# Optimization experiments

Measured on AMD Instinct MI355X. Metric: run time of the kernel, lower is better.

## Reference

```python
import jax, jax.numpy as jnp
import numpy as np

EMBED_DIM = 256
NUM_HEADS = 4
LN_EPS = 1e-5


def setup_inputs() -> dict:
    b, n, e = 2, 4096, EMBED_DIM
    key = jax.random.key(0)
    ks = jax.random.split(key, 12)
    x = jax.random.normal(ks[0], (b, n, e), dtype=jnp.float32)
    # rotary cache: cos/sin of random angles, shape [2, b, n, e, 1]
    ang = jax.random.uniform(ks[1], (b, n, e, 1), dtype=jnp.float32) * (2 * np.pi)
    encoding = jnp.stack([jnp.cos(ang), jnp.sin(ang)], axis=0)
    s_e = 1.0 / np.sqrt(e)
    s_2e = 1.0 / np.sqrt(2 * e)
    Wqkv_w = jax.random.normal(ks[2], (3 * e, e), dtype=jnp.float32) * s_e
    Wqkv_b = jax.random.normal(ks[3], (3 * e,), dtype=jnp.float32) * s_e
    out_w = jax.random.normal(ks[4], (e, e), dtype=jnp.float32) * s_e
    out_b = jax.random.normal(ks[5], (e,), dtype=jnp.float32) * s_e
    ffn1_w = jax.random.normal(ks[6], (2 * e, 2 * e), dtype=jnp.float32) * s_2e
    ffn1_b = jax.random.normal(ks[7], (2 * e,), dtype=jnp.float32) * s_2e
    ln_g = jnp.ones((2 * e,), dtype=jnp.float32)
    ln_b = jnp.zeros((2 * e,), dtype=jnp.float32)
    ffn2_w = jax.random.normal(ks[8], (e, 2 * e), dtype=jnp.float32) * s_2e
    ffn2_b = jax.random.normal(ks[9], (e,), dtype=jnp.float32) * s_2e
    return {"x": x, "encoding": encoding, "Wqkv_w": Wqkv_w, "Wqkv_b": Wqkv_b,
            "out_w": out_w, "out_b": out_b, "ffn1_w": ffn1_w, "ffn1_b": ffn1_b,
            "ln_g": ln_g, "ln_b": ln_b, "ffn2_w": ffn2_w, "ffn2_b": ffn2_b}


def _forward(x, encoding, Wqkv_w, Wqkv_b, out_w, out_b, ffn1_w, ffn1_b, ln_g, ln_b, ffn2_w, ffn2_b):
    b, n, e = x.shape
    h = NUM_HEADS
    hd = e // h
    qkv = x @ Wqkv_w.T + Wqkv_b                      # [b,n,3e]
    qkv = qkv.reshape(b, n, e, 3)
    qk, v = qkv[..., :2], qkv[..., 2]                # [b,n,e,2], [b,n,e]
    # rotate_half: interpret e as (h, hd//2, 2) pairs, rotate within pairs
    r = qk.reshape(b, n, h, hd // 2, 2, 2)
    r = jnp.stack([-r[..., 1, :], r[..., 0, :]], axis=4).reshape(b, n, e, 2)
    qk = qk * encoding[0] + r * encoding[1]          # cached rotary emb
    q = qk[..., 0].reshape(b, n, h, hd)
    k = qk[..., 1].reshape(b, n, h, hd)
    vh = v.reshape(b, n, h, hd)
    scale = 1.0 / np.sqrt(hd).astype(np.float32)
    scores = jnp.einsum('bqhd,bkhd->bhqk', q, k) * scale
    attn = jax.nn.softmax(scores, axis=-1)
    ctx = jnp.einsum('bhqk,bkhd->bqhd', attn, vh).reshape(b, n, e)
    message = ctx @ out_w.T + out_b
    y = jnp.concatenate([x, message], axis=2)        # [b,n,2e]
    y = y @ ffn1_w.T + ffn1_b
    mu = jnp.mean(y, axis=-1, keepdims=True)
    var = jnp.mean(jnp.square(y - mu), axis=-1, keepdims=True)
    y = (y - mu) * jax.lax.rsqrt(var + LN_EPS) * ln_g + ln_b
    y = jax.nn.gelu(y, approximate=False)            # torch nn.GELU default = exact
    y = y @ ffn2_w.T + ffn2_b
    return x + y


def reference(x, encoding, Wqkv_w, Wqkv_b, out_w, out_b, ffn1_w, ffn1_b, ln_g, ln_b, ffn2_w, ffn2_b):
    return _forward(x, encoding, Wqkv_w, Wqkv_b, out_w, out_b, ffn1_w, ffn1_b, ln_g, ln_b, ffn2_w, ffn2_b)
```

## Files before the change

kernel.cpp:

```cpp
#include <hip/hip_runtime.h>
#include <hip/hip_bf16.h>

using u16 = unsigned short;
using u16x8 = __attribute__((ext_vector_type(8))) unsigned short;
using s16x4 = __attribute__((ext_vector_type(4))) short;
using s16x8 = __attribute__((ext_vector_type(8))) short;
using f32x4 = __attribute__((ext_vector_type(4))) float;

__device__ __forceinline__ f32x4 mfma16(s16x8 a, s16x8 b, f32x4 c) {
    return __builtin_amdgcn_mfma_f32_16x16x32_bf16(a, b, c, 0, 0, 0);
}

__device__ __forceinline__ u16 f2bf(float f) {
    union { float f; unsigned u; } v; v.f = f;
    unsigned r = v.u + 0x7FFFu + ((v.u >> 16) & 1u);
    return (u16)(r >> 16);
}

__device__ __forceinline__ unsigned cvt_pk_bf16(float lo, float hi) {
    unsigned r;
    asm("v_cvt_pk_bf16_f32 %0, %1, %2" : "=v"(r) : "v"(lo), "v"(hi));
    return r;
}

__device__ __forceinline__ float fast_exp2(float x) {
    float r;
    asm("v_exp_f32 %0, %1" : "=v"(r) : "v"(x));
    return r;
}

__device__ __forceinline__ unsigned pk2(u16 a, u16 b) {
    return (unsigned)a | ((unsigned)b << 16);
}

__device__ __forceinline__ float bf2f(u16 u) {
    union { unsigned u; float f; } v; v.u = ((unsigned)u) << 16;
    return v.f;
}

__device__ __forceinline__ void gload_lds16(const u16* g, u16* l) {
    __builtin_amdgcn_global_load_lds(
        (const __attribute__((address_space(1))) void*)g,
        (__attribute__((address_space(3))) void*)l, 16, 0, 0);
}

__global__ __launch_bounds__(256) void conv_kernel(
    const float* __restrict__ s0, const float* __restrict__ s1,
    const float* __restrict__ s2, const float* __restrict__ s3,
    const float* __restrict__ s4,
    u16* __restrict__ d0, u16* __restrict__ d1, u16* __restrict__ d2,
    u16* __restrict__ d3, u16* __restrict__ d4)
{
    int i = blockIdx.x * 256 + threadIdx.x;
    const float* s; u16* d; int off;
    if (i < 524288)      { s = s0; d = d0; off = i; }
    else if (i < 573440) { s = s1; d = d1; off = i - 524288; }
    else if (i < 589824) { s = s2; d = d2; off = i - 573440; }
    else if (i < 655360) { s = s3; d = d3; off = i - 589824; }
    else                 { s = s4; d = d4; off = i - 655360; }
    float4 f = ((const float4*)s)[off];
    ushort4 u;
    u.x = f2bf(f.x); u.y = f2bf(f.y); u.z = f2bf(f.z); u.w = f2bf(f.w);
    ((ushort4*)d)[off] = u;
}

template<int OUTMODE, bool SPLIT, bool RESID>
__global__ __launch_bounds__(256) void gemm_kernel(
    const u16* __restrict__ A0, const u16* __restrict__ A1,
    const u16* __restrict__ W, const float* __restrict__ bias,
    const float* __restrict__ resid, float* __restrict__ outf,
    u16* __restrict__ outb, int M, int N, int K)
{
    __shared__ u16 A_lds[128][72];
    __shared__ u16 B_lds[64][72];
    const int tid = threadIdx.x;
    const int l = tid & 63, w = tid >> 6;
    const int lr = l & 15, lg = l >> 4;
    const int m0 = blockIdx.x * 128, n0 = blockIdx.y * 64;
    const int wm = (w >> 1) * 64, wn = (w & 1) * 32;

    f32x4 acc[4][2];
    #pragma unroll
    for (int i = 0; i < 4; ++i)
        #pragma unroll
        for (int j = 0; j < 2; ++j)
            acc[i][j] = (f32x4){0.f, 0.f, 0.f, 0.f};

    for (int k0 = 0; k0 < K; k0 += 64) {
        __syncthreads();
        const u16* Asrc; int lda;
        if (SPLIT) {
            lda = 256;
            Asrc = (k0 < 256) ? (A0 + k0) : (A1 + (k0 - 256));
        } else {
            lda = K; Asrc = A0 + k0;
        }
        #pragma unroll
        for (int i = 0; i < 4; ++i) {
            int c = tid + 256 * i;
            int row = c >> 3, cg = c & 7;
            *(uint4*)&A_lds[row][cg * 8] =
                *(const uint4*)(Asrc + (size_t)(m0 + row) * lda + cg * 8);
        }
        #pragma unroll
        for (int i = 0; i < 2; ++i) {
            int c = tid + 256 * i;
            int row = c >> 3, cg = c & 7;
            *(uint4*)&B_lds[row][cg * 8] =
                *(const uint4*)(W + (size_t)(n0 + row) * K + k0 + cg * 8);
        }
        __syncthreads();
        #pragma unroll
        for (int ks = 0; ks < 2; ++ks) {
            s16x8 af[4], bfr[2];
            #pragma unroll
            for (int ms = 0; ms < 4; ++ms)
                af[ms] = *(const s16x8*)&A_lds[wm + ms * 16 + lr][ks * 32 + lg * 8];
            #pragma unroll
            for (int ns = 0; ns < 2; ++ns)
                bfr[ns] = *(const s16x8*)&B_lds[wn + ns * 16 + lr][ks * 32 + lg * 8];
            #pragma unroll
            for (int ms = 0; ms < 4; ++ms)
                #pragma unroll
                for (int ns = 0; ns < 2; ++ns)
                    acc[ms][ns] = mfma16(af[ms], bfr[ns], acc[ms][ns]);
        }
    }
    #pragma unroll
    for (int ms = 0; ms < 4; ++ms) {
        #pragma unroll
        for (int ns = 0; ns < 2; ++ns) {
            int cg = n0 + wn + ns * 16 + lr;
            float bv = bias[cg];
            #pragma unroll
            for (int r = 0; r < 4; ++r) {
                int rg = m0 + wm + ms * 16 + lg * 4 + r;
                float val = acc[ms][ns][r] + bv;
                if (RESID) val += resid[(size_t)rg * N + cg];
                if (OUTMODE == 0) outf[(size_t)rg * N + cg] = val;
                else              outb[(size_t)rg * N + cg] = f2bf(val);
            }
        }
    }
}

__global__ __launch_bounds__(256) void rope_kernel(
    const u16* __restrict__ qkv, const float* __restrict__ enc,
    u16* __restrict__ Qo, u16* __restrict__ Ko, u16* __restrict__ Vo)
{
    int idx = blockIdx.x * 256 + threadIdx.x;
    int row = idx >> 7;
    int p = idx & 127;
    int c0 = p * 2;
    const u16* base = qkv + (size_t)row * 768 + p * 6;
    ushort2 a01 = *(const ushort2*)(base);
    ushort2 a23 = *(const ushort2*)(base + 2);
    ushort2 a45 = *(const ushort2*)(base + 4);
    float q0 = bf2f(a01.x), k0 = bf2f(a01.y);
    float q1 = bf2f(a23.y), k1 = bf2f(a45.x);
    const float* cb = enc + (size_t)row * 256 + c0;
    float2 cosv = *(const float2*)cb;
    float2 sinv = *(const float2*)(cb + 2097152);
    float qr0 = q0 * cosv.x - q1 * sinv.x;
    float qr1 = q1 * cosv.y + q0 * sinv.y;
    float kr0 = k0 * cosv.x - k1 * sinv.x;
    float kr1 = k1 * cosv.y + k0 * sinv.y;
    const float qs = 0.18033688011112042f;
    qr0 *= qs; qr1 *= qs;
    int h = c0 >> 6, d = c0 & 63;
    int b = row >> 12, n = row & 4095;
    size_t o = (((size_t)(b * 4 + h)) * 4096 + n) * 64 + d;
    *(unsigned*)(Qo + o) = cvt_pk_bf16(qr0, qr1);
    *(unsigned*)(Ko + o) = cvt_pk_bf16(kr0, kr1);
    *(unsigned*)(Vo + o) = pk2(a23.x, a45.y);
}

__global__ __launch_bounds__(256) void transpose_v(
    const u16* __restrict__ V, u16* __restrict__ Vt)
{
    __shared__ u16 t[64][72];
    int bh = blockIdx.y, n0 = blockIdx.x * 64;
    int tid = threadIdx.x;
    #pragma unroll
    for (int i = 0; i < 2; ++i) {
        int c = tid + 256 * i;
        int r = c >> 3, cg = c & 7;
        *(uint4*)&t[r][cg * 8] =
            *(const uint4*)(V + ((size_t)bh * 4096 + n0 + r) * 64 + cg * 8);
    }
    __syncthreads();
    #pragma unroll
    for (int i = 0; i < 2; ++i) {
        int c = tid + 256 * i;
        int d = c >> 3, ng = c & 7;
        unsigned w0 = pk2(t[ng*8+0][d], t[ng*8+1][d]);
        unsigned w1 = pk2(t[ng*8+2][d], t[ng*8+3][d]);
        unsigned w2 = pk2(t[ng*8+4][d], t[ng*8+5][d]);
        unsigned w3 = pk2(t[ng*8+6][d], t[ng*8+7][d]);
        uint4 o4 = make_uint4(w0, w1, w2, w3);
        *(uint4*)(Vt + ((size_t)bh * 64 + d) * 4096 + n0 + ng * 8) = o4;
    }
}

__global__ __launch_bounds__(256) void attn_kernel(
    const u16* __restrict__ Qp, const u16* __restrict__ Kp,
    const u16* __restrict__ Vtp, u16* __restrict__ Opart,
    float* __restrict__ Ssum)
{
    __shared__ u16 K_lds[2][64][64];
    __shared__ u16 V_lds[2][64][64];
    const int tid = threadIdx.x;
    const int l = tid & 63, w = tid >> 6;
    const int lr = l & 15, lg = l >> 4;
    const int bh = blockIdx.y, z = blockIdx.z;
    const int n0 = blockIdx.x * 64 + w * 16;

    const u16* Qb = Qp + ((size_t)bh * 4096 + n0) * 64;
    s16x8 qf0 = *(const s16x8*)(Qb + lr * 64 + lg * 8);
    s16x8 qf1 = *(const s16x8*)(Qb + lr * 64 + 32 + lg * 8);

    const u16* Kb = Kp + (size_t)bh * 4096 * 64 + (size_t)z * 1024 * 64;
    const u16* Vb = Vtp + (size_t)bh * 64 * 4096 + z * 1024;

    const int swz = (l & 7) ^ ((l >> 3) & 7);
    const int row0 = 16 * w + (l >> 3);
    const size_t koff0 = (size_t)row0 * 64 + swz * 8;
    const size_t koff1 = (size_t)(row0 + 8) * 64 + swz * 8;
    const size_t voff0 = (size_t)row0 * 4096 + swz * 8;
    const size_t voff1 = (size_t)(row0 + 8) * 4096 + swz * 8;

    #define STAGE(kt, b)                                                      \
        do {                                                                  \
            const u16* ks_ = Kb + (size_t)(kt) * 4096;                        \
            const u16* vs_ = Vb + (size_t)(kt) * 64;                          \
            gload_lds16(ks_ + koff0, &K_lds[b][16 * w][0]);                   \
            gload_lds16(ks_ + koff1, &K_lds[b][16 * w + 8][0]);               \
            gload_lds16(vs_ + voff0, &V_lds[b][16 * w][0]);                   \
            gload_lds16(vs_ + voff1, &V_lds[b][16 * w + 8][0]);               \
        } while (0)

    f32x4 O[4];
    #pragma unroll
    for (int dv = 0; dv < 4; ++dv) O[dv] = (f32x4){0.f, 0.f, 0.f, 0.f};
    f32x4 ssum = (f32x4){0.f, 0.f, 0.f, 0.f};
    s16x8 ones;
    #pragma unroll
    for (int j = 0; j < 8; ++j) ones[j] = (short)0x3F80;

    const int r7 = lr & 7;

    STAGE(0, 0);
    __syncthreads();

    for (int kt = 0; kt < 16; ++kt) {
        const int cur = kt & 1;
        if (kt + 1 < 16) STAGE(kt + 1, cur ^ 1);

        f32x4 S[4];
        #pragma unroll
        for (int v4 = 0; v4 < 4; ++v4) {
            const int krow = v4 * 16 + lr;
            s16x8 kf0 = *(const s16x8*)&K_lds[cur][krow][(lg ^ r7) * 8];
            s16x8 kf1 = *(const s16x8*)&K_lds[cur][krow][((4 + lg) ^ r7) * 8];
            f32x4 zz = (f32x4){-24.f, -24.f, -24.f, -24.f};
            zz = mfma16(kf0, qf0, zz);
            zz = mfma16(kf1, qf1, zz);
            S[v4] = zz;
        }

        float p[4][4];
        #pragma unroll
        for (int v4 = 0; v4 < 4; ++v4)
            #pragma unroll
            for (int r = 0; r < 4; ++r)
                p[v4][r] = fast_exp2(S[v4][r]);

        s16x8 pa[2];
        #pragma unroll
        for (int kb = 0; kb < 2; ++kb) {
            union { unsigned u[4]; s16x8 v; } pu;
            pu.u[0] = cvt_pk_bf16(p[2*kb][0],   p[2*kb][1]);
            pu.u[1] = cvt_pk_bf16(p[2*kb][2],   p[2*kb][3]);
            pu.u[2] = cvt_pk_bf16(p[2*kb+1][0], p[2*kb+1][1]);
            pu.u[3] = cvt_pk_bf16(p[2*kb+1][2], p[2*kb+1][3]);
            pa[kb] = pu.v;
        }

        #pragma unroll
        for (int dv = 0; dv < 4; ++dv) {
            const int vrow = 16 * dv + lr;
            #pragma unroll
            for (int kb = 0; kb < 2; ++kb) {
                const int c16a = 4 * kb + (lg >> 1);
                const u16* vpa = &V_lds[cur][vrow][((c16a      ^ r7) * 8) + 4 * (lg & 1)];
                const u16* vpb = &V_lds[cur][vrow][(((c16a + 2) ^ r7) * 8) + 4 * (lg & 1)];
                s16x4 va  = *(const s16x4*)vpa;
                s16x4 vb4 = *(const s16x4*)vpb;
                s16x8 vf = __builtin_shufflevector(va, vb4, 0,1,2,3,4,5,6,7);
                O[dv] = mfma16(pa[kb], vf, O[dv]);
            }
        }
        ssum = mfma16(pa[0], ones, ssum);
        ssum = mfma16(pa[1], ones, ssum);

        __syncthreads();
    }
    #undef STAGE

    u16* Ob = Opart + ((size_t)(z * 8 + bh) * 4096 + n0) * 64;
    #pragma unroll
    for (int dv = 0; dv < 4; ++dv)
        #pragma unroll
        for (int r = 0; r < 4; ++r)
            Ob[(size_t)(4 * lg + r) * 64 + 16 * dv + lr] = f2bf(O[dv][r]);
    if (lr == 0) {
        float4 sv = make_float4(ssum[0], ssum[1], ssum[2], ssum[3]);
        *(float4*)&Ssum[(size_t)(z * 8 + bh) * 4096 + n0 + 4 * lg] = sv;
    }
}

__global__ __launch_bounds__(256) void combine_kernel(
    const u16* __restrict__ Opart, const float* __restrict__ Ssum,
    u16* __restrict__ ctx)
{
    int idx = blockIdx.x * 256 + threadIdx.x;
    int rr = idx >> 3;
    int dc = (idx & 7) * 8;
    float s = Ssum[rr] + Ssum[32768 + rr] + Ssum[65536 + rr] + Ssum[98304 + rr];
    float inv = 1.f / s;
    float acc[8];
    #pragma unroll
    for (int j = 0; j < 8; ++j) acc[j] = 0.f;
    #pragma unroll
    for (int z = 0; z < 4; ++z) {
        u16x8 ov = *(const u16x8*)(Opart + ((size_t)z * 32768 + rr) * 64 + dc);
        #pragma unroll
        for (int j = 0; j < 8; ++j) acc[j] += bf2f(ov[j]);
    }
    #pragma unroll
    for (int j = 0; j < 8; ++j) acc[j] *= inv;
    int bh = rr >> 12, n = rr & 4095;
    int b = bh >> 2, h = bh & 3;
    uint4 o4 = make_uint4(cvt_pk_bf16(acc[0], acc[1]), cvt_pk_bf16(acc[2], acc[3]),
                          cvt_pk_bf16(acc[4], acc[5]), cvt_pk_bf16(acc[6], acc[7]));
    *(uint4*)(ctx + ((size_t)(b * 4096 + n)) * 256 + h * 64 + dc) = o4;
}

__global__ __launch_bounds__(256) void ln_gelu_kernel(
    const float* __restrict__ y, const float* __restrict__ g,
    const float* __restrict__ bta, u16* __restrict__ o)
{
    int row = blockIdx.x * 4 + (threadIdx.x >> 6);
    int l = threadIdx.x & 63;
    const float* yr = y + (size_t)row * 512 + l * 8;
    float4 va = *(const float4*)yr;
    float4 vb = *(const float4*)(yr + 4);
    float v[8] = {va.x, va.y, va.z, va.w, vb.x, vb.y, vb.z, vb.w};
    float s = 0.f;
    #pragma unroll
    for (int j = 0; j < 8; ++j) s += v[j];
    #pragma unroll
    for (int off = 32; off; off >>= 1) s += __shfl_xor(s, off, 64);
    float mu = s * (1.f / 512.f);
    float q = 0.f;
    #pragma unroll
    for (int j = 0; j < 8; ++j) { float t = v[j] - mu; q += t * t; }
    #pragma unroll
    for (int off = 32; off; off >>= 1) q += __shfl_xor(q, off, 64);
    float rs = rsqrtf(q * (1.f / 512.f) + 1e-5f);
    u16 u[8];
    #pragma unroll
    for (int j = 0; j < 8; ++j) {
        float t = (v[j] - mu) * rs * g[l * 8 + j] + bta[l * 8 + j];
        t = t * 0.5f * (1.f + erff(t * 0.70710678118654752f));
        u[j] = f2bf(t);
    }
    uint4 o4 = make_uint4(pk2(u[0], u[1]), pk2(u[2], u[3]),
                          pk2(u[4], u[5]), pk2(u[6], u[7]));
    *(uint4*)(o + (size_t)row * 512 + l * 8) = o4;
}

extern "C" void kernel_launch(void* const* d_in, const int* in_sizes, int n_in,
                              void* d_out, int out_size, void* d_ws, size_t ws_size,
                              hipStream_t stream) {
    (void)in_sizes; (void)n_in; (void)out_size; (void)ws_size;
    const float* x    = (const float*)d_in[0];
    const float* enc  = (const float*)d_in[1];
    const float* wqkv = (const float*)d_in[2];
    const float* bqkv = (const float*)d_in[3];
    const float* wout = (const float*)d_in[4];
    const float* bout = (const float*)d_in[5];
    const float* w1   = (const float*)d_in[6];
    const float* b1   = (const float*)d_in[7];
    const float* lng  = (const float*)d_in[8];
    const float* lnb  = (const float*)d_in[9];
    const float* w2   = (const float*)d_in[10];
    const float* b2   = (const float*)d_in[11];
    float* out = (float*)d_out;
    char* ws = (char*)d_ws;

    u16*   xb    = (u16*)(ws + 0);
    u16*   wqkvb = (u16*)(ws + 4194304);
    u16*   woutb = (u16*)(ws + 4587520);
    u16*   w1b   = (u16*)(ws + 4718592);
    u16*   w2b   = (u16*)(ws + 5242880);
    u16*   qkvb  = (u16*)(ws + 5505024);
    u16*   OpartB= (u16*)(ws + 5505024);
    float* y1    = (float*)(ws + 5505024);
    float* Ssum  = (float*)(ws + 22282240);
    u16*   q     = (u16*)(ws + 30670848);
    u16*   k     = (u16*)(ws + 34865152);
    u16*   v     = (u16*)(ws + 39059456);
    u16*   vt    = (u16*)(ws + 43253760);
    u16*   ybf   = q;
    u16*   ctx   = (u16*)(ws + 47448064);
    u16*   msg   = (u16*)(ws + 51642368);

    conv_kernel<<<2688, 256, 0, stream>>>(x, wqkv, wout, w1, w2,
                                          xb, wqkvb, woutb, w1b, w2b);
    gemm_kernel<1, false, false><<<dim3(64, 12), 256, 0, stream>>>(
        xb, nullptr, wqkvb, bqkv, nullptr, nullptr, qkvb, 8192, 768, 256);
    rope_kernel<<<4096, 256, 0, stream>>>(qkvb, enc, q, k, v);
    transpose_v<<<dim3(64, 8), 256, 0, stream>>>(v, vt);
    attn_kernel<<<dim3(64, 8, 4), 256, 0, stream>>>(q, k, vt, OpartB, Ssum);
    combine_kernel<<<1024, 256, 0, stream>>>(OpartB, Ssum, ctx);
    gemm_kernel<1, false, false><<<dim3(64, 4), 256, 0, stream>>>(
        ctx, nullptr, woutb, bout, nullptr, nullptr, msg, 8192, 256, 256);
    gemm_kernel<0, true, false><<<dim3(64, 8), 256, 0, stream>>>(
        xb, msg, w1b, b1, nullptr, y1, nullptr, 8192, 512, 512);
    ln_gelu_kernel<<<2048, 256, 0, stream>>>(y1, lng, lnb, ybf);
    gemm_kernel<0, false, true><<<dim3(64, 4), 256, 0, stream>>>(
        ybf, nullptr, w2b, b2, x, out, nullptr, 8192, 256, 512);
}
```

Before: 139.4 us.

## Triple-buffer LDS with async global-to-LDS loads in GEMM and attention

The GEMM kernel moves from synchronous register-staged loads with two barriers per k-step to direct global-to-LDS async loads into a 3-deep XOR-swizzled ring buffer, prefetching the next stage and using vmcnt waits plus a single barrier per iteration. The attention kernel goes from double to triple buffering of K/V tiles and drops the trailing barrier. The aim is to overlap memory latency with MFMA work and cut synchronisation. The cost is more LDS per block, which may lower occupancy. Correctness with one barrier also depends on the exact vmcnt counts and the ring depth.

New measurement: 135.3 us. -2.9%, faster.

```diff
diff --git a/kernel.cpp b/kernel.cpp
--- a/kernel.cpp
+++ b/kernel.cpp
@@ -71,14 +71,38 @@
     const float* __restrict__ resid, float* __restrict__ outf,
     u16* __restrict__ outb, int M, int N, int K)
 {
-    __shared__ u16 A_lds[128][72];
-    __shared__ u16 B_lds[64][72];
+    __shared__ u16 A_lds[3][128][64];
+    __shared__ u16 B_lds[3][64][64];
     const int tid = threadIdx.x;
     const int l = tid & 63, w = tid >> 6;
     const int lr = l & 15, lg = l >> 4;
+    const int r7 = lr & 7;
     const int m0 = blockIdx.x * 128, n0 = blockIdx.y * 64;
     const int wm = (w >> 1) * 64, wn = (w & 1) * 32;
 
+    const int lrow = l >> 3;
+    const int swz = (l & 7) ^ lrow;
+    const int arow = 32 * w + lrow;
+    const int brow = 16 * w + lrow;
+
+    #define STAGE_G(s, b)                                                     \
+        do {                                                                  \
+            int k0_ = 64 * (s);                                               \
+            const u16* As_; int lda_;                                         \
+            if (SPLIT) {                                                      \
+                lda_ = 256;                                                   \
+                As_ = (k0_ < 256) ? (A0 + k0_) : (A1 + (k0_ - 256));          \
+            } else { lda_ = K; As_ = A0 + k0_; }                              \
+            _Pragma("unroll")                                                 \
+            for (int i = 0; i < 4; ++i)                                       \
+                gload_lds16(As_ + (size_t)(m0 + arow + 8 * i) * lda_ + swz * 8,\
+                            &A_lds[b][32 * w + 8 * i][0]);                    \
+            _Pragma("unroll")                                                 \
+            for (int i = 0; i < 2; ++i)                                       \
+                gload_lds16(W + (size_t)(n0 + brow + 8 * i) * K + k0_ + swz * 8,\
+                            &B_lds[b][16 * w + 8 * i][0]);                    \
+        } while (0)
+
     f32x4 acc[4][2];
     #pragma unroll
     for (int i = 0; i < 4; ++i)
@@ -86,46 +110,43 @@
         for (int j = 0; j < 2; ++j)
             acc[i][j] = (f32x4){0.f, 0.f, 0.f, 0.f};
 
-    for (int k0 = 0; k0 < K; k0 += 64) {
-        __syncthreads();
-        const u16* Asrc; int lda;
-        if (SPLIT) {
-            lda = 256;
-            Asrc = (k0 < 256) ? (A0 + k0) : (A1 + (k0 - 256));
+    const int NS = K >> 6;
+    int cur = 0, nxt = 1;
+    STAGE_G(0, 0);
+
+    for (int s = 0; s < NS; ++s) {
+        if (s + 1 < NS) {
+            STAGE_G(s + 1, nxt);
+            asm volatile("s_waitcnt vmcnt(6)" ::: "memory");
         } else {
-            lda = K; Asrc = A0 + k0;
-        }
-        #pragma unroll
-        for (int i = 0; i < 4; ++i) {
-            int c = tid + 256 * i;
-            int row = c >> 3, cg = c & 7;
-            *(uint4*)&A_lds[row][cg * 8] =
-                *(const uint4*)(Asrc + (size_t)(m0 + row) * lda + cg * 8);
-        }
-        #pragma unroll
-        for (int i = 0; i < 2; ++i) {
-            int c = tid + 256 * i;
-            int row = c >> 3, cg = c & 7;
-            *(uint4*)&B_lds[row][cg * 8] =
-                *(const uint4*)(W + (size_t)(n0 + row) * K + k0 + cg * 8);
-        }
-        __syncthreads();
+            asm volatile("s_waitcnt vmcnt(0)" ::: "memory");
+        }
+        __builtin_amdgcn_sched_barrier(0);
+        __builtin_amdgcn_s_barrier();
+        __builtin_amdgcn_sched_barrier(0);
+
         #pragma unroll
         for (int ks = 0; ks < 2; ++ks) {
             s16x8 af[4], bfr[2];
             #pragma unroll
             for (int ms = 0; ms < 4; ++ms)
-                af[ms] = *(const s16x8*)&A_lds[wm + ms * 16 + lr][ks * 32 + lg * 8];
+                af[ms] = *(const s16x8*)&A_lds[cur][wm + ms * 16 + lr]
+                                              [((ks * 4 + lg) ^ r7) * 8];
             #pragma unroll
             for (int ns = 0; ns < 2; ++ns)
-                bfr[ns] = *(const s16x8*)&B_lds[wn + ns * 16 + lr][ks * 32 + lg * 8];
+                bfr[ns] = *(const s16x8*)&B_lds[cur][wn + ns * 16 + lr]
+                                               [((ks * 4 + lg) ^ r7) * 8];
             #pragma unroll
             for (int ms = 0; ms < 4; ++ms)
                 #pragma unroll
                 for (int ns = 0; ns < 2; ++ns)
                     acc[ms][ns] = mfma16(af[ms], bfr[ns], acc[ms][ns]);
         }
-    }
+        cur = nxt;
+        nxt = (nxt == 2) ? 0 : nxt + 1;
+    }
+    #undef STAGE_G
+
     #pragma unroll
     for (int ms = 0; ms < 4; ++ms) {
         #pragma unroll
@@ -207,8 +228,8 @@
     const u16* __restrict__ Vtp, u16* __restrict__ Opart,
     float* __restrict__ Ssum)
 {
-    __shared__ u16 K_lds[2][64][64];
-    __shared__ u16 V_lds[2][64][64];
+    __shared__ u16 K_lds[3][64][64];
+    __shared__ u16 V_lds[3][64][64];
     const int tid = threadIdx.x;
     const int l = tid & 63, w = tid >> 6;
     const int lr = l & 15, lg = l >> 4;
@@ -248,13 +269,19 @@
     for (int j = 0; j < 8; ++j) ones[j] = (short)0x3F80;
 
     const int r7 = lr & 7;
-
+    int cur = 0, nxt = 1;
     STAGE(0, 0);
-    __syncthreads();
 
     for (int kt = 0; kt < 16; ++kt) {
-        const int cur = kt & 1;
-        if (kt + 1 < 16) STAGE(kt + 1, cur ^ 1);
+        if (kt + 1 < 16) {
+            STAGE(kt + 1, nxt);
+            asm volatile("s_waitcnt vmcnt(4)" ::: "memory");
+        } else {
+            asm volatile("s_waitcnt vmcnt(0)" ::: "memory");
+        }
+        __builtin_amdgcn_sched_barrier(0);
+        __builtin_amdgcn_s_barrier();
+        __builtin_amdgcn_sched_barrier(0);
 
         f32x4 S[4];
         #pragma unroll
@@ -303,7 +330,8 @@
         ssum = mfma16(pa[0], ones, ssum);
         ssum = mfma16(pa[1], ones, ssum);
 
-        __syncthreads();
+        cur = nxt;
+        nxt = (nxt == 2) ? 0 : nxt + 1;
     }
     #undef STAGE
 
```
